# Optimization experiments

Measured on AMD Instinct MI355X. Metric: run time of the kernel, lower is better.

Reference implementation:

```python
import jax, jax.numpy as jnp
import numpy as np

N, E, DIN, DH, HEADS, DOUT = 50000, 800000, 128, 32, 4, 16
NL_HID = 2  # num_layers - 1
HID = HEADS * DH


def setup_inputs() -> dict:
    key = jax.random.key(0)
    ks = jax.random.split(key, 16)

    def w(k, shape, fan_in):
        return jax.random.normal(k, shape, jnp.float32) * (1.0 / np.sqrt(fan_in))

    return {
        "x": jax.random.normal(ks[0], (N, DIN), jnp.float32),
        "edge_index": jax.random.randint(ks[1], (2, E), 0, N, dtype=jnp.int64),
        "edge_attr": jax.random.normal(ks[2], (E, 1), jnp.float32),
        # conv1: dim_in -> (heads, dim_h)
        "W1": w(ks[3], (DIN, HID), DIN),
        "as1": w(ks[4], (HEADS, DH), DH),
        "ad1": w(ks[5], (HEADS, DH), DH),
        "b1": jnp.zeros((HID,), jnp.float32),
        # hidden convs: hid -> (heads, dim_h), stacked over NL_HID layers
        "Wh": w(ks[6], (NL_HID, HID, HID), HID),
        "ash": w(ks[7], (NL_HID, HEADS, DH), DH),
        "adh": w(ks[8], (NL_HID, HEADS, DH), DH),
        "bh": jnp.zeros((NL_HID, HID), jnp.float32),
        # conv2: hid -> (1, dim_out)
        "W2": w(ks[9], (HID, DOUT), HID),
        "as2": w(ks[10], (1, DOUT), DOUT),
        "ad2": w(ks[11], (1, DOUT), DOUT),
        "b2": jnp.zeros((DOUT,), jnp.float32),
    }


def _gat_conv(x, src, dst, W, a_s, a_d, b):
    """PyG GATConv (eval mode: attention dropout inactive), concat heads."""
    H, C = a_s.shape
    n = x.shape[0]
    h = (x @ W).reshape(n, H, C)                       # [N,H,C]
    al_s = jnp.einsum('nhc,hc->nh', h, a_s)            # [N,H]
    al_d = jnp.einsum('nhc,hc->nh', h, a_d)
    e = jax.nn.leaky_relu(al_s[src] + al_d[dst], 0.2)  # [Et,H]
    # scatter-softmax over incoming edges of each destination node
    m = jax.ops.segment_max(e, dst, num_segments=n)
    ee = jnp.exp(e - m[dst])
    denom = jax.ops.segment_sum(ee, dst, num_segments=n)
    alpha = ee / (denom[dst] + 1e-16)                  # [Et,H]
    out = jax.ops.segment_sum(h[src] * alpha[:, :, None], dst, num_segments=n)
    return out.reshape(n, H * C) + b


def reference(x, edge_index, edge_attr, W1, as1, ad1, b1, Wh, ash, adh, bh, W2, as2, ad2, b2):
    n = x.shape[0]
    # GATConv adds self-loops by default
    loops = jnp.arange(n, dtype=edge_index.dtype)
    src = jnp.concatenate([edge_index[0], loops])
    dst = jnp.concatenate([edge_index[1], loops])
    h = jax.nn.elu(_gat_conv(x, src, dst, W1, as1, ad1, b1))
    for i in range(Wh.shape[0]):  # dropout p=0.5 inactive in eval mode
        h = jax.nn.elu(_gat_conv(h, src, dst, Wh[i], ash[i], adh[i], bh[i]))
    return _gat_conv(h, src, dst, W2, as2, ad2, b2)  # heads=1 -> [N, DOUT]
```

## Files before the change

kernel.cpp:

```cpp
#include <hip/hip_runtime.h>
#include <hip/hip_bf16.h>
#include <hip/hip_fp16.h>


typedef _Float16 half8_t __attribute__((ext_vector_type(8)));
typedef float f32x4_t  __attribute__((ext_vector_type(4)));

static inline int divup(int a, int b){ return (a + b - 1) / b; }


__global__ __launch_bounds__(256) void zero_cnt_kernel(int* __restrict__ cnt, int n){
    int i = blockIdx.x * 256 + threadIdx.x;
    int4 z = {0, 0, 0, 0};
    if (i * 4 + 3 < n){
        *(int4*)(cnt + i * 4) = z;
    } else {
        for (int j = i * 4; j < n; ++j) cnt[j] = 0;
    }
}


__global__ __launch_bounds__(256) void fill_sliced_kernel(const int* __restrict__ src,
                                                          const int* __restrict__ dst,
                                                          int* __restrict__ cnt,
                                                          unsigned short* __restrict__ csr,
                                                          int E, int Et){
    int slice = blockIdx.x & 7;
    int e = (blockIdx.x >> 3) * 256 + threadIdx.x;
    if (e >= Et) return;
    int d = (e < E) ? dst[e] : (e - E);
    if (((d >> 4) & 7) != slice) return;
    int s = (e < E) ? src[e] : d;
    int pos = atomicAdd(&cnt[d], 1);
    csr[(d << 6) + pos] = (unsigned short)s;
}


__global__ __launch_bounds__(256) void prep_kernel(const float* __restrict__ W1,
                                                   const float* __restrict__ Wh,
                                                   const float* __restrict__ as1,
                                                   const float* __restrict__ ad1,
                                                   const float* __restrict__ ash,
                                                   const float* __restrict__ adh,
                                                   const float* __restrict__ W2,
                                                   const float* __restrict__ as2,
                                                   const float* __restrict__ ad2,
                                                   _Float16* __restrict__ WTx,
                                                   _Float16* __restrict__ W2x){
    int id = blockIdx.x * 256 + threadIdx.x;
    const int MAIN = 3 * 144 * 128;
    if (id < MAIN){
        int l = id / (144 * 128), rem = id % (144 * 128);
        int c = rem >> 7, k = rem & 127;
        const float* W = (l == 0) ? W1 : (Wh + (size_t)(l - 1) * 16384);
        float v = 0.f;
        if (c < 128){
            v = W[k * 128 + c];
        } else if (c < 136){
            int h = (c - 128) & 3;
            const float* a = (c < 132) ? ((l == 0) ? as1 : ash + (size_t)(l - 1) * 128)
                                       : ((l == 0) ? ad1 : adh + (size_t)(l - 1) * 128);
            const float* wr = W + k * 128 + h * 32;
            const float* ar = a + h * 32;
            float sum = 0.f;
            #pragma unroll
            for (int c2 = 0; c2 < 32; ++c2) sum += wr[c2] * ar[c2];
            v = sum;
        }
        WTx[id] = (_Float16)v;
    } else if (id < MAIN + 32 * 128){
        int id2 = id - MAIN;
        int c = id2 >> 7, k = id2 & 127;
        float v = 0.f;
        if (c < 16){
            v = W2[k * 16 + c];
        } else if (c == 16 || c == 17){
            const float* a = (c == 16) ? as2 : ad2;
            float sum = 0.f;
            #pragma unroll
            for (int j = 0; j < 16; ++j) sum += W2[k * 16 + j] * a[j];
            v = sum;
        }
        W2x[id2] = (_Float16)v;
    }
}


template<bool F32IN>
__device__ __forceinline__ void gemm128L_body(const void* __restrict__ Xv,
                                              const _Float16* __restrict__ WTx,
                                              _Float16* __restrict__ H16,
                                              float* __restrict__ als,
                                              float* __restrict__ ald, int n){
    int wav = threadIdx.x >> 6, lane = threadIdx.x & 63;
    int nb = blockIdx.x * 16;
    int r = lane & 15, kg = lane >> 4;
    int anode = nb + r; if (anode >= n) anode = n - 1;

    half8_t a0, a1, a2, a3;
    if (F32IN){
        const float* xrow = (const float*)Xv + (size_t)anode * 128 + kg * 8;
        #pragma unroll
        for (int q = 0; q < 4; ++q){
            float4 u = *(const float4*)(xrow + q * 32);
            float4 w = *(const float4*)(xrow + q * 32 + 4);
            half8_t o = {(_Float16)u.x,(_Float16)u.y,(_Float16)u.z,(_Float16)u.w,
                         (_Float16)w.x,(_Float16)w.y,(_Float16)w.z,(_Float16)w.w};
            if (q == 0) a0 = o; else if (q == 1) a1 = o; else if (q == 2) a2 = o; else a3 = o;
        }
    } else {
        const _Float16* xrow = (const _Float16*)Xv + (size_t)anode * 128 + kg * 8;
        a0 = *(const half8_t*)(xrow);
        a1 = *(const half8_t*)(xrow + 32);
        a2 = *(const half8_t*)(xrow + 64);
        a3 = *(const half8_t*)(xrow + 96);
    }

    const _Float16* wc0 = WTx + (size_t)(wav * 32 + r) * 128 + kg * 8;
    const _Float16* wc1 = wc0 + 16 * 128;

    f32x4_t c0 = {0.f,0.f,0.f,0.f}, c1 = {0.f,0.f,0.f,0.f};
    c0 = __builtin_amdgcn_mfma_f32_16x16x32_f16(a0, *(const half8_t*)(wc0     ), c0, 0,0,0);
    c1 = __builtin_amdgcn_mfma_f32_16x16x32_f16(a0, *(const half8_t*)(wc1     ), c1, 0,0,0);
    c0 = __builtin_amdgcn_mfma_f32_16x16x32_f16(a1, *(const half8_t*)(wc0 + 32), c0, 0,0,0);
    c1 = __builtin_amdgcn_mfma_f32_16x16x32_f16(a1, *(const half8_t*)(wc1 + 32), c1, 0,0,0);
    c0 = __builtin_amdgcn_mfma_f32_16x16x32_f16(a2, *(const half8_t*)(wc0 + 64), c0, 0,0,0);
    c1 = __builtin_amdgcn_mfma_f32_16x16x32_f16(a2, *(const half8_t*)(wc1 + 64), c1, 0,0,0);
    c0 = __builtin_amdgcn_mfma_f32_16x16x32_f16(a3, *(const half8_t*)(wc0 + 96), c0, 0,0,0);
    c1 = __builtin_amdgcn_mfma_f32_16x16x32_f16(a3, *(const half8_t*)(wc1 + 96), c1, 0,0,0);

    int colw = wav * 32 + r;
    #pragma unroll
    for (int rg = 0; rg < 4; ++rg){
        int onode = nb + kg * 4 + rg;
        if (onode < n){
            _Float16* hr = H16 + (size_t)onode * 128 + colw;
            hr[0]  = (_Float16)c0[rg];
            hr[16] = (_Float16)c1[rg];
        }
    }

    if (wav == 0){
        const _Float16* wl = WTx + (size_t)(128 + r) * 128 + kg * 8;
        f32x4_t cl = {0.f,0.f,0.f,0.f};
        cl = __builtin_amdgcn_mfma_f32_16x16x32_f16(a0, *(const half8_t*)(wl     ), cl, 0,0,0);
        cl = __builtin_amdgcn_mfma_f32_16x16x32_f16(a1, *(const half8_t*)(wl + 32), cl, 0,0,0);
        cl = __builtin_amdgcn_mfma_f32_16x16x32_f16(a2, *(const half8_t*)(wl + 64), cl, 0,0,0);
        cl = __builtin_amdgcn_mfma_f32_16x16x32_f16(a3, *(const half8_t*)(wl + 96), cl, 0,0,0);
        if (r < 8){
            #pragma unroll
            for (int rg = 0; rg < 4; ++rg){
                int onode = nb + kg * 4 + rg;
                if (onode < n){
                    if (r < 4) als[(size_t)onode * 4 + r]       = cl[rg];
                    else       ald[(size_t)onode * 4 + (r - 4)] = cl[rg];
                }
            }
        }
    }
}

__global__ __launch_bounds__(256) void gemm128L_f32_kernel(const float* __restrict__ X,
                                                           const _Float16* __restrict__ WTx,
                                                           _Float16* __restrict__ H16,
                                                           float* __restrict__ als,
                                                           float* __restrict__ ald, int n){
    gemm128L_body<true>(X, WTx, H16, als, ald, n);
}

__global__ __launch_bounds__(256) void gemm128L_f16_kernel(const _Float16* __restrict__ X16,
                                                           const _Float16* __restrict__ WTx,
                                                           _Float16* __restrict__ H16,
                                                           float* __restrict__ als,
                                                           float* __restrict__ ald, int n){
    gemm128L_body<false>(X16, WTx, H16, als, ald, n);
}


__global__ __launch_bounds__(256) void gemm16L_kernel(const _Float16* __restrict__ X16,
                                                      const _Float16* __restrict__ W2x,
                                                      _Float16* __restrict__ H4,
                                                      float* __restrict__ als4,
                                                      float* __restrict__ ald4, int n){
    int wav = threadIdx.x >> 6, lane = threadIdx.x & 63;
    int nb = blockIdx.x * 64 + wav * 16;
    int r = lane & 15, kg = lane >> 4;
    int anode = nb + r; if (anode >= n) anode = n - 1;

    const _Float16* xrow = X16 + (size_t)anode * 128 + kg * 8;
    half8_t a0 = *(const half8_t*)(xrow);
    half8_t a1 = *(const half8_t*)(xrow + 32);
    half8_t a2 = *(const half8_t*)(xrow + 64);
    half8_t a3 = *(const half8_t*)(xrow + 96);

    const _Float16* wc0 = W2x + (size_t)r * 128 + kg * 8;
    const _Float16* wc1 = wc0 + 16 * 128;

    f32x4_t c0 = {0.f,0.f,0.f,0.f}, c1 = {0.f,0.f,0.f,0.f};
    c0 = __builtin_amdgcn_mfma_f32_16x16x32_f16(a0, *(const half8_t*)(wc0     ), c0, 0,0,0);
    c1 = __builtin_amdgcn_mfma_f32_16x16x32_f16(a0, *(const half8_t*)(wc1     ), c1, 0,0,0);
    c0 = __builtin_amdgcn_mfma_f32_16x16x32_f16(a1, *(const half8_t*)(wc0 + 32), c0, 0,0,0);
    c1 = __builtin_amdgcn_mfma_f32_16x16x32_f16(a1, *(const half8_t*)(wc1 + 32), c1, 0,0,0);
    c0 = __builtin_amdgcn_mfma_f32_16x16x32_f16(a2, *(const half8_t*)(wc0 + 64), c0, 0,0,0);
    c1 = __builtin_amdgcn_mfma_f32_16x16x32_f16(a2, *(const half8_t*)(wc1 + 64), c1, 0,0,0);
    c0 = __builtin_amdgcn_mfma_f32_16x16x32_f16(a3, *(const half8_t*)(wc0 + 96), c0, 0,0,0);
    c1 = __builtin_amdgcn_mfma_f32_16x16x32_f16(a3, *(const half8_t*)(wc1 + 96), c1, 0,0,0);

    #pragma unroll
    for (int rg = 0; rg < 4; ++rg){
        int onode = nb + kg * 4 + rg;
        if (onode < n){
            H4[(size_t)onode * 16 + r] = (_Float16)c0[rg];
            if (r == 0) als4[onode] = c1[rg];
            else if (r == 1) ald4[onode] = c1[rg];
        }
    }
}


__global__ __launch_bounds__(256) void aggregate128_kernel(const __half* __restrict__ H16,
                                                           const float* __restrict__ als,
                                                           const float* __restrict__ ald,
                                                           const int* __restrict__ cnt,
                                                           const unsigned short* __restrict__ csr,
                                                           const float* __restrict__ bias,
                                                           _Float16* __restrict__ out16,
                                                           int n){
    int node = blockIdx.x * 4 + (threadIdx.x >> 6);
    int lane = threadIdx.x & 63;
    if (node >= n) return;
    int start = node << 6;
    int deg = cnt[node];
    int end = start + deg;

    int eg = lane >> 4, cl = lane & 15;
    int h = cl >> 2;
    float ad_h = ald[(size_t)node * 4 + h];

    float den = 0.f;
    float acc[8] = {0,0,0,0,0,0,0,0};
    const __half* Hc = H16 + cl * 8;
    int i = start + eg;
    for (; i + 4 < end; i += 8){
        int sA = csr[i];
        int sB = csr[i + 4];
        float eA = als[(size_t)sA * 4 + h] + ad_h; eA = eA > 0.f ? eA : 0.2f * eA;
        float eB = als[(size_t)sB * 4 + h] + ad_h; eB = eB > 0.f ? eB : 0.2f * eB;
        float wA = __expf(eA);
        float wB = __expf(eB);
        den += wA + wB;
        uint4 ra = *(const uint4*)(Hc + (size_t)sA * 128);
        uint4 rb = *(const uint4*)(Hc + (size_t)sB * 128);
        float2 a0 = __half22float2(*(__half2*)&ra.x);
        float2 a1 = __half22float2(*(__half2*)&ra.y);
        float2 a2 = __half22float2(*(__half2*)&ra.z);
        float2 a3 = __half22float2(*(__half2*)&ra.w);
        float2 b0 = __half22float2(*(__half2*)&rb.x);
        float2 b1 = __half22float2(*(__half2*)&rb.y);
        float2 b2 = __half22float2(*(__half2*)&rb.z);
        float2 b3 = __half22float2(*(__half2*)&rb.w);
        acc[0] += wA * a0.x + wB * b0.x; acc[1] += wA * a0.y + wB * b0.y;
        acc[2] += wA * a1.x + wB * b1.x; acc[3] += wA * a1.y + wB * b1.y;
        acc[4] += wA * a2.x + wB * b2.x; acc[5] += wA * a2.y + wB * b2.y;
        acc[6] += wA * a3.x + wB * b3.x; acc[7] += wA * a3.y + wB * b3.y;
    }
    if (i < end){
        int s = csr[i];
        float e = als[(size_t)s * 4 + h] + ad_h; e = e > 0.f ? e : 0.2f * e;
        float w = __expf(e);
        den += w;
        uint4 ra = *(const uint4*)(Hc + (size_t)s * 128);
        float2 a0 = __half22float2(*(__half2*)&ra.x);
        float2 a1 = __half22float2(*(__half2*)&ra.y);
        float2 a2 = __half22float2(*(__half2*)&ra.z);
        float2 a3 = __half22float2(*(__half2*)&ra.w);
        acc[0] += w * a0.x; acc[1] += w * a0.y;
        acc[2] += w * a1.x; acc[3] += w * a1.y;
        acc[4] += w * a2.x; acc[5] += w * a2.y;
        acc[6] += w * a3.x; acc[7] += w * a3.y;
    }
    #pragma unroll
    for (int j = 0; j < 8; ++j){
        acc[j] += __shfl_xor(acc[j], 16);
        acc[j] += __shfl_xor(acc[j], 32);
    }
    den += __shfl_xor(den, 16);
    den += __shfl_xor(den, 32);

    if (eg == 0){
        float inv = 1.f / (den + 1e-16f);
        int col = cl * 8;
        float4 bv0 = *(const float4*)(bias + col);
        float4 bv1 = *(const float4*)(bias + col + 4);
        float v[8];
        v[0] = acc[0]*inv + bv0.x; v[1] = acc[1]*inv + bv0.y;
        v[2] = acc[2]*inv + bv0.z; v[3] = acc[3]*inv + bv0.w;
        v[4] = acc[4]*inv + bv1.x; v[5] = acc[5]*inv + bv1.y;
        v[6] = acc[6]*inv + bv1.z; v[7] = acc[7]*inv + bv1.w;
        #pragma unroll
        for (int j = 0; j < 8; ++j) v[j] = v[j] > 0.f ? v[j] : __expf(v[j]) - 1.f;

        half8_t o16 = {(_Float16)v[0], (_Float16)v[1], (_Float16)v[2], (_Float16)v[3],
                       (_Float16)v[4], (_Float16)v[5], (_Float16)v[6], (_Float16)v[7]};
        *(half8_t*)&out16[(size_t)node * 128 + col] = o16;
    }
}


__global__ __launch_bounds__(256) void aggregate16_kernel(const _Float16* __restrict__ H4,
                                                          const float* __restrict__ als4,
                                                          const float* __restrict__ ald4,
                                                          const int* __restrict__ cnt,
                                                          const unsigned short* __restrict__ csr,
                                                          const float* __restrict__ bias,
                                                          float* __restrict__ out, int n){
    int node = blockIdx.x * 4 + (threadIdx.x >> 6);
    int lane = threadIdx.x & 63;
    if (node >= n) return;
    int start = node << 6, deg = cnt[node];
    float adn = ald4[node];

    int eg = lane >> 2, cl = lane & 3;
    float den = 0.f;
    float acc0 = 0.f, acc1 = 0.f, acc2 = 0.f, acc3 = 0.f;
    for (int i = eg; i < deg; i += 16){
        int s = csr[start + i];
        float e = als4[s] + adn; e = e > 0.f ? e : 0.2f * e;
        float w = __expf(e);
        den += w;
        uint2 hv = *(const uint2*)(H4 + (size_t)s * 16 + cl * 4);
        float2 h0 = __half22float2(*(__half2*)&hv.x);
        float2 h1 = __half22float2(*(__half2*)&hv.y);
        acc0 += w * h0.x; acc1 += w * h0.y; acc2 += w * h1.x; acc3 += w * h1.y;
    }
    #pragma unroll
    for (int off = 4; off <= 32; off <<= 1){
        acc0 += __shfl_xor(acc0, off); acc1 += __shfl_xor(acc1, off);
        acc2 += __shfl_xor(acc2, off); acc3 += __shfl_xor(acc3, off);
        den  += __shfl_xor(den,  off);
    }

    if (eg == 0){
        float inv = 1.f / (den + 1e-16f);
        float4 bv = *(const float4*)(bias + cl * 4);
        float4 o = {acc0*inv + bv.x, acc1*inv + bv.y, acc2*inv + bv.z, acc3*inv + bv.w};
        *(float4*)&out[(size_t)node * 16 + cl * 4] = o;
    }
}


extern "C" void kernel_launch(void* const* d_in, const int* in_sizes, int n_in,
                              void* d_out, int out_size, void* d_ws, size_t ws_size,
                              hipStream_t stream) {
    const float* x   = (const float*)d_in[0];
    const int*   ei  = (const int*)d_in[1];
    const float* W1  = (const float*)d_in[3];
    const float* as1 = (const float*)d_in[4];
    const float* ad1 = (const float*)d_in[5];
    const float* b1  = (const float*)d_in[6];
    const float* Wh  = (const float*)d_in[7];
    const float* ash = (const float*)d_in[8];
    const float* adh = (const float*)d_in[9];
    const float* bh  = (const float*)d_in[10];
    const float* W2  = (const float*)d_in[11];
    const float* as2 = (const float*)d_in[12];
    const float* ad2 = (const float*)d_in[13];
    const float* b2  = (const float*)d_in[14];

    int N = in_sizes[0] / 128;
    int E = in_sizes[1] / 2;
    int Et = E + N;
    const int* srcA = ei;
    const int* dstA = ei + E;

    char* ws = (char*)d_ws;
    size_t off = 0;
    auto alloc = [&](size_t bytes) -> void* {
        void* p = ws + off;
        off = (off + bytes + 255) & ~(size_t)255;
        return p;
    };
    int* cnt      = (int*)alloc((size_t)N * 4);
    unsigned short* csr = (unsigned short*)alloc((size_t)N * 64 * 2);
    _Float16* xbuf16 = (_Float16*)alloc((size_t)N * 128 * 2);
    _Float16* h16    = (_Float16*)alloc((size_t)N * 128 * 2);
    _Float16* wtx    = (_Float16*)alloc((size_t)3 * 144 * 128 * 2);
    _Float16* w2x    = (_Float16*)alloc((size_t)32 * 128 * 2);
    float* als_a  = (float*)alloc((size_t)N * 4 * 4);
    float* ald_a  = (float*)alloc((size_t)N * 4 * 4);
    _Float16* h4  = (_Float16*)alloc((size_t)N * 16 * 2);
    float* als4   = (float*)alloc((size_t)N * 4);
    float* ald4   = (float*)alloc((size_t)N * 4);

    zero_cnt_kernel<<<divup(divup(N, 4), 256), 256, 0, stream>>>(cnt, N);
    prep_kernel<<<divup(3 * 144 * 128 + 32 * 128, 256), 256, 0, stream>>>(
        W1, Wh, as1, ad1, ash, adh, W2, as2, ad2, wtx, w2x);
    fill_sliced_kernel<<<divup(Et, 256) * 8, 256, 0, stream>>>(srcA, dstA, cnt, csr, E, Et);

    float* out = (float*)d_out;
    const size_t WSTRIDE = (size_t)144 * 128;

    gemm128L_f32_kernel<<<divup(N, 16), 256, 0, stream>>>(x, wtx, h16, als_a, ald_a, N);
    aggregate128_kernel<<<divup(N, 4), 256, 0, stream>>>((const __half*)h16, als_a, ald_a, cnt, csr,
                                                        b1, xbuf16, N);
    gemm128L_f16_kernel<<<divup(N, 16), 256, 0, stream>>>(xbuf16, wtx + WSTRIDE, h16, als_a, ald_a, N);
    aggregate128_kernel<<<divup(N, 4), 256, 0, stream>>>((const __half*)h16, als_a, ald_a, cnt, csr,
                                                        bh, xbuf16, N);
    gemm128L_f16_kernel<<<divup(N, 16), 256, 0, stream>>>(xbuf16, wtx + 2 * WSTRIDE, h16, als_a, ald_a, N);
    aggregate128_kernel<<<divup(N, 4), 256, 0, stream>>>((const __half*)h16, als_a, ald_a, cnt, csr,
                                                        bh + 128, xbuf16, N);

    gemm16L_kernel<<<divup(N, 64), 256, 0, stream>>>(xbuf16, w2x, h4, als4, ald4, N);
    aggregate16_kernel<<<divup(N, 4), 256, 0, stream>>>(h4, als4, ald4, cnt, csr, b2, out, N);
}
```

Measured before the change: 258.6 us.

## Split 128-wide aggregation into per-head blocks with nontemporal CSR loads

```diff
diff --git a/kernel.cpp b/kernel.cpp
--- a/kernel.cpp
+++ b/kernel.cpp
@@ -218,15 +218,16 @@
 }
 
 
-__global__ __launch_bounds__(256) void aggregate128_kernel(const __half* __restrict__ H16,
-                                                           const float* __restrict__ als,
-                                                           const float* __restrict__ ald,
-                                                           const int* __restrict__ cnt,
-                                                           const unsigned short* __restrict__ csr,
-                                                           const float* __restrict__ bias,
-                                                           _Float16* __restrict__ out16,
-                                                           int n){
-    int node = blockIdx.x * 4 + (threadIdx.x >> 6);
+__global__ __launch_bounds__(256) void aggregate128q_kernel(const _Float16* __restrict__ H16,
+                                                            const float* __restrict__ als,
+                                                            const float* __restrict__ ald,
+                                                            const int* __restrict__ cnt,
+                                                            const unsigned short* __restrict__ csr,
+                                                            const float* __restrict__ bias,
+                                                            _Float16* __restrict__ out16,
+                                                            int n){
+    int q = blockIdx.x & 3;
+    int node = (blockIdx.x >> 2) * 4 + (threadIdx.x >> 6);
     int lane = threadIdx.x & 63;
     if (node >= n) return;
     int start = node << 6;
@@ -234,75 +235,49 @@
     int end = start + deg;
 
     int eg = lane >> 4, cl = lane & 15;
-    int h = cl >> 2;
-    float ad_h = ald[(size_t)node * 4 + h];
-
-    float den = 0.f;
-    float acc[8] = {0,0,0,0,0,0,0,0};
-    const __half* Hc = H16 + cl * 8;
+    float ad_h = ald[(size_t)node * 4 + q];
+
+    float den = 0.f, accx = 0.f, accy = 0.f;
+    const _Float16* Hq = H16 + q * 32 + cl * 2;
     int i = start + eg;
     for (; i + 4 < end; i += 8){
-        int sA = csr[i];
-        int sB = csr[i + 4];
-        float eA = als[(size_t)sA * 4 + h] + ad_h; eA = eA > 0.f ? eA : 0.2f * eA;
-        float eB = als[(size_t)sB * 4 + h] + ad_h; eB = eB > 0.f ? eB : 0.2f * eB;
+        int sA = __builtin_nontemporal_load(&csr[i]);
+        int sB = __builtin_nontemporal_load(&csr[i + 4]);
+        float eA = als[(size_t)sA * 4 + q] + ad_h; eA = eA > 0.f ? eA : 0.2f * eA;
+        float eB = als[(size_t)sB * 4 + q] + ad_h; eB = eB > 0.f ? eB : 0.2f * eB;
         float wA = __expf(eA);
         float wB = __expf(eB);
         den += wA + wB;
-        uint4 ra = *(const uint4*)(Hc + (size_t)sA * 128);
-        uint4 rb = *(const uint4*)(Hc + (size_t)sB * 128);
-        float2 a0 = __half22float2(*(__half2*)&ra.x);
-        float2 a1 = __half22float2(*(__half2*)&ra.y);
-        float2 a2 = __half22float2(*(__half2*)&ra.z);
-        float2 a3 = __half22float2(*(__half2*)&ra.w);
-        float2 b0 = __half22float2(*(__half2*)&rb.x);
-        float2 b1 = __half22float2(*(__half2*)&rb.y);
-        float2 b2 = __half22float2(*(__half2*)&rb.z);
-        float2 b3 = __half22float2(*(__half2*)&rb.w);
-        acc[0] += wA * a0.x + wB * b0.x; acc[1] += wA * a0.y + wB * b0.y;
-        acc[2] += wA * a1.x + wB * b1.x; acc[3] += wA * a1.y + wB * b1.y;
-        acc[4] += wA * a2.x + wB * b2.x; acc[5] += wA * a2.y + wB * b2.y;
-        acc[6] += wA * a3.x + wB * b3.x; acc[7] += wA * a3.y + wB * b3.y;
+        unsigned int ua = *(const unsigned int*)(Hq + (size_t)sA * 128);
+        unsigned int ub = *(const unsigned int*)(Hq + (size_t)sB * 128);
+        float2 fa = __half22float2(*(__half2*)&ua);
+        float2 fb = __half22float2(*(__half2*)&ub);
+        accx += wA * fa.x + wB * fb.x;
+        accy += wA * fa.y + wB * fb.y;
     }
     if (i < end){
-        int s = csr[i];
-        float e = als[(size_t)s * 4 + h] + ad_h; e = e > 0.f ? e : 0.2f * e;
+        int s = __builtin_nontemporal_load(&csr[i]);
+        float e = als[(size_t)s * 4 + q] + ad_h; e = e > 0.f ? e : 0.2f * e;
         float w = __expf(e);
         den += w;
-        uint4 ra = *(const uint4*)(Hc + (size_t)s * 128);
-        float2 a0 = __half22float2(*(__half2*)&ra.x);
-        float2 a1 = __half22float2(*(__half2*)&ra.y);
-        float2 a2 = __half22float2(*(__half2*)&ra.z);
-        float2 a3 = __half22float2(*(__half2*)&ra.w);
-        acc[0] += w * a0.x; acc[1] += w * a0.y;
-        acc[2] += w * a1.x; acc[3] += w * a1.y;
-        acc[4] += w * a2.x; acc[5] += w * a2.y;
-        acc[6] += w * a3.x; acc[7] += w * a3.y;
-    }
-    #pragma unroll
-    for (int j = 0; j < 8; ++j){
-        acc[j] += __shfl_xor(acc[j], 16);
-        acc[j] += __shfl_xor(acc[j], 32);
-    }
-    den += __shfl_xor(den, 16);
-    den += __shfl_xor(den, 32);
+        unsigned int ua = *(const unsigned int*)(Hq + (size_t)s * 128);
+        float2 fa = __half22float2(*(__half2*)&ua);
+        accx += w * fa.x; accy += w * fa.y;
+    }
+    accx += __shfl_xor(accx, 16); accx += __shfl_xor(accx, 32);
+    accy += __shfl_xor(accy, 16); accy += __shfl_xor(accy, 32);
+    den  += __shfl_xor(den, 16);  den  += __shfl_xor(den, 32);
 
     if (eg == 0){
         float inv = 1.f / (den + 1e-16f);
-        int col = cl * 8;
-        float4 bv0 = *(const float4*)(bias + col);
-        float4 bv1 = *(const float4*)(bias + col + 4);
-        float v[8];
-        v[0] = acc[0]*inv + bv0.x; v[1] = acc[1]*inv + bv0.y;
-        v[2] = acc[2]*inv + bv0.z; v[3] = acc[3]*inv + bv0.w;
-        v[4] = acc[4]*inv + bv1.x; v[5] = acc[5]*inv + bv1.y;
-        v[6] = acc[6]*inv + bv1.z; v[7] = acc[7]*inv + bv1.w;
-        #pragma unroll
-        for (int j = 0; j < 8; ++j) v[j] = v[j] > 0.f ? v[j] : __expf(v[j]) - 1.f;
-
-        half8_t o16 = {(_Float16)v[0], (_Float16)v[1], (_Float16)v[2], (_Float16)v[3],
-                       (_Float16)v[4], (_Float16)v[5], (_Float16)v[6], (_Float16)v[7]};
-        *(half8_t*)&out16[(size_t)node * 128 + col] = o16;
+        int col = q * 32 + cl * 2;
+        float vx = accx * inv + bias[col];
+        float vy = accy * inv + bias[col + 1];
+        vx = vx > 0.f ? vx : __expf(vx) - 1.f;
+        vy = vy > 0.f ? vy : __expf(vy) - 1.f;
+        __half2 o = __floats2half2_rn(vx, vy);
+        __builtin_nontemporal_store(*(unsigned int*)&o,
+                                    (unsigned int*)(out16 + (size_t)node * 128 + col));
     }
 }
 
@@ -399,15 +374,16 @@
 
     float* out = (float*)d_out;
     const size_t WSTRIDE = (size_t)144 * 128;
+    int aggq_grid = divup(N, 4) * 4;
 
     gemm128L_f32_kernel<<<divup(N, 16), 256, 0, stream>>>(x, wtx, h16, als_a, ald_a, N);
-    aggregate128_kernel<<<divup(N, 4), 256, 0, stream>>>((const __half*)h16, als_a, ald_a, cnt, csr,
+    aggregate128q_kernel<<<aggq_grid, 256, 0, stream>>>(h16, als_a, ald_a, cnt, csr,
                                                         b1, xbuf16, N);
     gemm128L_f16_kernel<<<divup(N, 16), 256, 0, stream>>>(xbuf16, wtx + WSTRIDE, h16, als_a, ald_a, N);
-    aggregate128_kernel<<<divup(N, 4), 256, 0, stream>>>((const __half*)h16, als_a, ald_a, cnt, csr,
+    aggregate128q_kernel<<<aggq_grid, 256, 0, stream>>>(h16, als_a, ald_a, cnt, csr,
                                                         bh, xbuf16, N);
     gemm128L_f16_kernel<<<divup(N, 16), 256, 0, stream>>>(xbuf16, wtx + 2 * WSTRIDE, h16, als_a, ald_a, N);
-    aggregate128_kernel<<<divup(N, 4), 256, 0, stream>>>((const __half*)h16, als_a, ald_a, cnt, csr,
+    aggregate128q_kernel<<<aggq_grid, 256, 0, stream>>>(h16, als_a, ald_a, cnt, csr,
                                                         bh + 128, xbuf16, N);
 
     gemm16L_kernel<<<divup(N, 64), 256, 0, stream>>>(xbuf16, w2x, h4, als4, ald4, N);
```

Measured after the change: 492.3 us. 90.4% more time.
